# Kernel tuning notes

Hardware: AMD Instinct MI355X
Metric: run time of the kernel (lower is better)

The kernel has to match this reference:

```python
import jax, jax.numpy as jnp
import numpy as np

B = 131072
DIM = 64
D_IN = 32
D_OUT = 32
HIDDEN = 512
N_BINS = 8
TAIL = 3.0


def setup_inputs() -> dict:
    key = jax.random.key(0)
    ks = jax.random.split(key, 7)
    x = jax.random.normal(ks[0], (B, DIM), dtype=jnp.float32)
    out_dim = D_OUT * (3 * N_BINS - 1)  # 32 * 23 = 736
    W1 = jax.random.normal(ks[1], (D_IN, HIDDEN), dtype=jnp.float32) / np.sqrt(D_IN)
    b1 = jnp.zeros((HIDDEN,), dtype=jnp.float32)
    W2 = jax.random.normal(ks[2], (HIDDEN, HIDDEN), dtype=jnp.float32) / np.sqrt(HIDDEN)
    b2 = jnp.zeros((HIDDEN,), dtype=jnp.float32)
    W3 = jax.random.normal(ks[3], (HIDDEN, out_dim), dtype=jnp.float32) / np.sqrt(HIDDEN)
    b3 = jnp.zeros((out_dim,), dtype=jnp.float32)
    return {"x": x, "W1": W1, "b1": b1, "W2": W2, "b2": b2, "W3": W3, "b3": b3}


def _gather(t, idx):
    # t: (..., K), idx: (...) -> (...,)
    return jnp.take_along_axis(t, idx[..., None], axis=-1)[..., 0]


def rq_spline_forward(x, widths, heights, derivatives, tail_bound=TAIL):
    K = widths.shape[-1]
    widths = jax.nn.softmax(widths, axis=-1) * 2 * tail_bound
    heights = jax.nn.softmax(heights, axis=-1) * 2 * tail_bound
    derivatives = jax.nn.softplus(derivatives)
    ones = jnp.ones_like(derivatives[..., :1])
    derivatives = jnp.concatenate([ones, derivatives, ones], axis=-1)  # (..., K+1)
    cumwidths = jnp.cumsum(widths, axis=-1)
    cumwidths = jnp.pad(cumwidths, [(0, 0)] * (cumwidths.ndim - 1) + [(1, 0)]) - tail_bound
    cumheights = jnp.cumsum(heights, axis=-1)
    cumheights = jnp.pad(cumheights, [(0, 0)] * (cumheights.ndim - 1) + [(1, 0)]) - tail_bound

    inside = (x >= -tail_bound) & (x <= tail_bound)
    xc = jnp.clip(x, -tail_bound + 1e-6, tail_bound - 1e-6)
    # searchsorted (left): number of knots strictly less than xc
    bin_idx = jnp.sum(cumwidths[..., 1:] < xc[..., None], axis=-1)
    bin_idx = jnp.clip(bin_idx, 0, K - 1)

    w_k = _gather(widths, bin_idx)
    h_k = _gather(heights, bin_idx)
    d_k = _gather(derivatives, bin_idx)
    d_k1 = _gather(derivatives[..., 1:], bin_idx)
    cw_k = _gather(cumwidths, bin_idx)
    ch_k = _gather(cumheights, bin_idx)

    xi = jnp.clip((xc - cw_k) / w_k, 1e-6, 1 - 1e-6)
    s_k = h_k / w_k
    num = h_k * (s_k * xi**2 + d_k * xi * (1 - xi))
    den = s_k + (d_k + d_k1 - 2 * s_k) * xi * (1 - xi)
    y_inside = ch_k + num / den
    log_det_inside = (
        jnp.log(s_k**2 * (d_k1 * xi**2 + 2 * s_k * xi * (1 - xi) + d_k * (1 - xi) ** 2) + 1e-8)
        - jnp.log(den**2 + 1e-8)
    )
    y = jnp.where(inside, y_inside, x)
    log_det = jnp.where(inside, log_det_inside, jnp.zeros_like(x))
    return y, log_det


def reference(x, W1, b1, W2, b2, W3, b3):
    # mask: first D_IN dims conditioned on, last D_OUT transformed
    x_masked = x[:, :D_IN]
    x_transform = x[:, D_IN:]
    h = jax.nn.relu(x_masked @ W1 + b1)
    h = jax.nn.relu(h @ W2 + b2)
    raw = h @ W3 + b3
    raw = raw.reshape(x.shape[0], D_OUT, 3 * N_BINS - 1)
    widths = raw[..., :N_BINS]
    heights = raw[..., N_BINS:2 * N_BINS]
    derivs = raw[..., 2 * N_BINS:]
    y_t, log_det = rq_spline_forward(x_transform, widths, heights, derivs, TAIL)
    y = jnp.concatenate([x_masked, y_t], axis=-1)
    return y, jnp.sum(log_det, axis=-1)
```

## Files before the change

### kernel.cpp

```cpp
#include <hip/hip_runtime.h>
#include <hip/hip_bf16.h>
#include <stdint.h>

typedef __bf16 bf16_t;
typedef _Float16 f16_t;
typedef _Float16 f16x8 __attribute__((ext_vector_type(8)));
typedef _Float16 f16x4 __attribute__((ext_vector_type(4)));
typedef float f32x4 __attribute__((ext_vector_type(4)));

#define HID 512
#define NRAW 736
#define NRAW_PAD 768
#define TAILB 3.0f

__device__ __forceinline__ void glds16(const void* g, void* s) {
  __builtin_amdgcn_global_load_lds(
      (const __attribute__((address_space(1))) void*)g,
      (__attribute__((address_space(3))) void*)s, 16, 0, 0);
}
__device__ __forceinline__ float frcp(float x) { return __builtin_amdgcn_rcpf(x); }

__global__ void detect_dtype(const void* x, int* flag) {
  __shared__ int s;
  if (threadIdx.x == 0) s = 0;
  __syncthreads();
  const bf16_t* xb = (const bf16_t*)x;
  int cnt = 0;
  for (int j = 0; j < 16; j++) {
    float v = (float)xb[threadIdx.x * 16 + j];
    if (!(v == v) || fabsf(v) > 64.0f) cnt++;
  }
  atomicAdd(&s, cnt);
  __syncthreads();
  if (threadIdx.x == 0) *flag = (s > 64) ? 1 : 0;
}

__global__ void conv_wb(const void* W1, const void* W2, const void* W3,
                        const void* b1, const void* b2, const void* b3,
                        f16_t* __restrict__ w1t, f16_t* __restrict__ w2t,
                        f16_t* __restrict__ w3t,
                        float* __restrict__ bf1, float* __restrict__ bf2,
                        float* __restrict__ bf3, const int* flagp) {
  const int flag = *flagp;
  auto rd = [&](const void* p, size_t idx) -> float {
    return flag ? ((const float*)p)[idx] : (float)((const bf16_t*)p)[idx];
  };
  int i = blockIdx.x * 256 + threadIdx.x;
  if (i < 512 * 32)  { w1t[i] = (f16_t)rd(W1, (size_t)(i & 31) * 512 + (i >> 5)); return; }
  i -= 512 * 32;
  if (i < 512 * 512) { w2t[i] = (f16_t)rd(W2, (size_t)(i & 511) * 512 + (i >> 9)); return; }
  i -= 512 * 512;
  if (i < NRAW_PAD * 512) {
    int n = i >> 9, k = i & 511;
    int ch = n / 24, e = n % 24;
    w3t[i] = (e < 23) ? (f16_t)rd(W3, (size_t)k * NRAW + ch * 23 + e) : (f16_t)0.0f;
    return;
  }
  i -= NRAW_PAD * 512;
  if (i < 512) { bf1[i] = rd(b1, i); return; }
  i -= 512;
  if (i < 512) { bf2[i] = rd(b2, i); return; }
  i -= 512;
  if (i < NRAW_PAD) {
    int ch = i / 24, e = i % 24;
    bf3[i] = (e < 23) ? rd(b3, (size_t)ch * 23 + e) : 0.0f;
  }
}

__global__ void convert_x(const void* x, void* __restrict__ outv,
                          const int* flagp, int n) {
  const int flag = *flagp;
  const int i0 = (blockIdx.x * 256 + threadIdx.x) * 8;
  if (i0 >= n) return;
  const int row = i0 >> 5, col = i0 & 31;
  const size_t src = (size_t)row * 64 + col;
  if (flag) {
    const float4* s4 = (const float4*)((const float*)x + src);
    float4* d4 = (float4*)((float*)outv + src);
    d4[0] = s4[0]; d4[1] = s4[1];
  } else {
    *(uint4*)((bf16_t*)outv + src) = *(const uint4*)((const bf16_t*)x + src);
  }
}

__global__ void ld_finalize(const float* __restrict__ ldp, void* __restrict__ outv,
                            const int* __restrict__ flagp, int M) {
  const int i = blockIdx.x * 256 + threadIdx.x;
  if (i >= M) return;
  float s = 0.f;
  #pragma unroll
  for (int n = 0; n < 8; n++) s += ldp[(size_t)n * M + i];
  if (*flagp) ((float*)outv)[(size_t)M * 64 + i] = s;
  else        ((bf16_t*)outv)[(size_t)M * 64 + i] = (bf16_t)s;
}

__launch_bounds__(256)
__global__ void gemm12(const void* __restrict__ xorig, const f16_t* __restrict__ W1t,
                       const float* __restrict__ b1, const f16_t* __restrict__ W2t,
                       const float* __restrict__ b2, f16_t* __restrict__ H2,
                       int r0, const int* __restrict__ flagp) {
  constexpr int BK = 64;
  __shared__ __align__(16) f16_t As[128 * BK], Bs[128 * BK];
  const int t = threadIdx.x;
  const int id = blockIdx.x;
  const int xcd = id & 7, s = id >> 3;
  const int n0 = (s & 3) * 128;
  const int m0 = ((s >> 2) * 8 + xcd) * 128;
  const int lrow = t >> 3, lcb = t & 7;
  const int lane = t & 63, w = t >> 6;
  const int wr = (w >> 1) * 64, wc = (w & 1) * 64, wc2 = (w & 1) * 32;
  const int lm = lane & 15, quad = lane >> 4;
  const int flag = *flagp;

  const f16_t* gb[4];
  f16_t* ldb[4];
  #pragma unroll
  for (int r = 0; r < 4; r++) {
    const int row = r * 32 + lrow;
    const int gc = (lcb ^ (row & 7)) * 8;
    gb[r] = W2t + (size_t)(n0 + row) * 512 + gc;
    ldb[r] = &Bs[row * BK + lcb * 8];
  }
  const f16x8* ap[4][2];
  const f16x8* bp[4][2];
  #pragma unroll
  for (int i = 0; i < 4; i++) {
    const int ra = wr + i * 16 + lm, rb = wc + i * 16 + lm;
    #pragma unroll
    for (int ksi = 0; ksi < 2; ksi++) {
      const int qb = ksi * 4 + quad;
      ap[i][ksi] = (const f16x8*)&As[ra * BK + ((qb ^ (ra & 7)) << 3)];
      bp[i][ksi] = (const f16x8*)&Bs[rb * BK + ((qb ^ (rb & 7)) << 3)];
    }
  }
  f16x8 xfr[4];
  #pragma unroll
  for (int i = 0; i < 4; i++) {
    const size_t xrow = (size_t)(r0 + m0 + wr + i * 16 + lm);
    if (flag) {
      const float* px = (const float*)xorig + xrow * 64 + quad * 8;
      const float4 a = *(const float4*)px;
      const float4 b = *(const float4*)(px + 4);
      f16x8 v;
      v[0] = (f16_t)a.x; v[1] = (f16_t)a.y; v[2] = (f16_t)a.z; v[3] = (f16_t)a.w;
      v[4] = (f16_t)b.x; v[5] = (f16_t)b.y; v[6] = (f16_t)b.z; v[7] = (f16_t)b.w;
      xfr[i] = v;
    } else {
      const bf16_t* px = (const bf16_t*)xorig + xrow * 64 + quad * 8;
      f16x8 v;
      #pragma unroll
      for (int j = 0; j < 8; j++) v[j] = (f16_t)(float)px[j];
      xfr[i] = v;
    }
  }
  const f16_t* w1p0 = W1t + (size_t)(wc2 + lm) * 32 + quad * 8;
  const f16_t* w1p1 = W1t + (size_t)(wc2 + 16 + lm) * 32 + quad * 8;
  const float* b1p0 = b1 + wc2 + 4 * quad;
  const float* b1p1 = b1 + wc2 + 16 + 4 * quad;
  f16_t* wadr[4][2];
  #pragma unroll
  for (int i = 0; i < 4; i++) {
    const int row = wr + i * 16 + lm;
    #pragma unroll
    for (int Tl = 0; Tl < 2; Tl++) {
      const int cb = (wc2 >> 3) + 2 * Tl + (quad >> 1);
      wadr[i][Tl] = &As[row * BK + ((cb ^ (row & 7)) << 3) + 4 * (quad & 1)];
    }
  }

  f32x4 acc[4][4] = {};
  f16x8 w1f0 = *(const f16x8*)w1p0;
  f16x8 w1f1 = *(const f16x8*)w1p1;

  #pragma unroll
  for (int k0i = 0; k0i < 8; k0i++) {
    const int k0 = k0i * 64;
    #pragma unroll
    for (int r = 0; r < 4; r++) glds16(gb[r] + k0, ldb[r]);
    const float4 bv0 = *(const float4*)(b1p0 + k0);
    const float4 bv1 = *(const float4*)(b1p1 + k0);
    f32x4 h[4][2];
    #pragma unroll
    for (int i = 0; i < 4; i++) {
      f32x4 z = {};
      h[i][0] = __builtin_amdgcn_mfma_f32_16x16x32_f16(w1f0, xfr[i], z, 0, 0, 0);
      h[i][1] = __builtin_amdgcn_mfma_f32_16x16x32_f16(w1f1, xfr[i], z, 0, 0, 0);
    }
    if (k0i < 7) {
      w1f0 = *(const f16x8*)(w1p0 + (size_t)(k0 + 64) * 32);
      w1f1 = *(const f16x8*)(w1p1 + (size_t)(k0 + 64) * 32);
    }
    __syncthreads();
    #pragma unroll
    for (int i = 0; i < 4; i++) {
      f16x4 v0, v1;
      v0[0] = (f16_t)fmaxf(h[i][0][0] + bv0.x, 0.0f);
      v0[1] = (f16_t)fmaxf(h[i][0][1] + bv0.y, 0.0f);
      v0[2] = (f16_t)fmaxf(h[i][0][2] + bv0.z, 0.0f);
      v0[3] = (f16_t)fmaxf(h[i][0][3] + bv0.w, 0.0f);
      v1[0] = (f16_t)fmaxf(h[i][1][0] + bv1.x, 0.0f);
      v1[1] = (f16_t)fmaxf(h[i][1][1] + bv1.y, 0.0f);
      v1[2] = (f16_t)fmaxf(h[i][1][2] + bv1.z, 0.0f);
      v1[3] = (f16_t)fmaxf(h[i][1][3] + bv1.w, 0.0f);
      *(f16x4*)wadr[i][0] = v0;
      *(f16x4*)wadr[i][1] = v1;
    }
    __syncthreads();
    #pragma unroll
    for (int ksi = 0; ksi < 2; ksi++) {
      f16x8 af[4], bf[4];
      #pragma unroll
      for (int i = 0; i < 4; i++) af[i] = *ap[i][ksi];
      #pragma unroll
      for (int j = 0; j < 4; j++) bf[j] = *bp[j][ksi];
      #pragma unroll
      for (int i = 0; i < 4; i++)
        #pragma unroll
        for (int j = 0; j < 4; j++)
          acc[i][j] = __builtin_amdgcn_mfma_f32_16x16x32_f16(af[i], bf[j], acc[i][j], 0, 0, 0);
    }
    if (k0i < 7) __syncthreads();
  }
  #pragma unroll
  for (int i = 0; i < 4; i++)
    #pragma unroll
    for (int j = 0; j < 4; j++) {
      const int col = n0 + wc + j * 16 + lm;
      const float bv = b2[col];
      #pragma unroll
      for (int r = 0; r < 4; r++) {
        const int rowi = m0 + wr + i * 16 + quad * 4 + r;
        H2[(size_t)rowi * HID + col] = (f16_t)fmaxf(acc[i][j][r] + bv, 0.0f);
      }
    }
}

#define RSH 104
#define SP1 0.5413248546f

__launch_bounds__(256)
__global__ void gemm3_spline(const f16_t* __restrict__ A, const f16_t* __restrict__ Bt,
                             const float* __restrict__ bias,
                             const void* __restrict__ xorig,
                             void* __restrict__ outv, float* __restrict__ ldp,
                             int M, int r0, const int* __restrict__ flagp) {
  constexpr int BK = 64;
  __shared__ __align__(16) char smem[16384 + 12288];
  f16_t* As = (f16_t*)smem;
  f16_t* Bs = (f16_t*)(smem + 16384);
  f16_t* rawh = (f16_t*)smem;

  const int t = threadIdx.x;
  const int id = blockIdx.x;
  const int xcd = id & 7, s = id >> 3;
  const int ntile = s & 7;
  const int m0 = ((s >> 3) * 8 + xcd) * 128;
  const int n0 = ntile * 96;
  const int lrow = t >> 3, lcb = t & 7;
  const int lane = t & 63, w = t >> 6;
  const int wr = (w >> 1) * 64, wc = (w & 1) * 48;
  const int lm = lane & 15, quad = lane >> 4;
  const int flag = *flagp;

  const int prow = t >> 2, pch = ntile * 4 + (t & 3);
  float xt_pre[2];
  #pragma unroll
  for (int e = 0; e < 2; e++) {
    const size_t gi = (size_t)(r0 + m0 + e * 64 + prow) * 64 + 32 + pch;
    xt_pre[e] = flag ? ((const float*)xorig)[gi] : (float)((const bf16_t*)xorig)[gi];
  }

  const f16_t* ga[4];
  const f16_t* gb[3];
  f16_t* lda[4];
  f16_t* ldb[3];
  #pragma unroll
  for (int r = 0; r < 4; r++) {
    const int row = r * 32 + lrow;
    const int gc = (lcb ^ (row & 7)) * 8;
    ga[r] = A + (size_t)(m0 + row) * 512 + gc;
    lda[r] = &As[row * BK + lcb * 8];
  }
  #pragma unroll
  for (int r = 0; r < 3; r++) {
    const int row = r * 32 + lrow;
    const int gc = (lcb ^ (row & 7)) * 8;
    gb[r] = Bt + (size_t)(n0 + row) * 512 + gc;
    ldb[r] = &Bs[row * BK + lcb * 8];
  }
  const f16x8* ap[4][2];
  const f16x8* bp[3][2];
  #pragma unroll
  for (int ksi = 0; ksi < 2; ksi++) {
    const int qb = ksi * 4 + quad;
    #pragma unroll
    for (int i = 0; i < 4; i++) {
      const int ra = wr + i * 16 + lm;
      ap[i][ksi] = (const f16x8*)&As[ra * BK + ((qb ^ (ra & 7)) << 3)];
    }
    #pragma unroll
    for (int j = 0; j < 3; j++) {
      const int rb = wc + j * 16 + lm;
      bp[j][ksi] = (const f16x8*)&Bs[rb * BK + ((qb ^ (rb & 7)) << 3)];
    }
  }

  f32x4 acc[4][3] = {};

  #pragma unroll
  for (int k0 = 0; k0 < 512; k0 += BK) {
    #pragma unroll
    for (int r = 0; r < 4; r++) glds16(ga[r] + k0, lda[r]);
    #pragma unroll
    for (int r = 0; r < 3; r++) glds16(gb[r] + k0, ldb[r]);
    __syncthreads();
    #pragma unroll
    for (int ksi = 0; ksi < 2; ksi++) {
      f16x8 af[4], bf[3];
      #pragma unroll
      for (int i = 0; i < 4; i++) af[i] = *ap[i][ksi];
      #pragma unroll
      for (int j = 0; j < 3; j++) bf[j] = *bp[j][ksi];
      #pragma unroll
      for (int i = 0; i < 4; i++)
        #pragma unroll
        for (int j = 0; j < 3; j++)
          acc[i][j] = __builtin_amdgcn_mfma_f32_16x16x32_f16(af[i], bf[j], acc[i][j], 0, 0, 0);
    }
    __syncthreads();
  }

  #pragma unroll
  for (int i = 0; i < 4; i++)
    #pragma unroll
    for (int j = 0; j < 3; j++) {
      const int col = wc + j * 16 + lm;
      const float bv = bias[n0 + col];
      #pragma unroll
      for (int r = 0; r < 4; r++)
        rawh[(wr + i * 16 + quad * 4 + r) * RSH + col] = (f16_t)(acc[i][j][r] + bv);
    }
  __syncthreads();

  #pragma unroll
  for (int e = 0; e < 2; e++) {
    const int row = e * 64 + prow;
    const f16_t* c16 = &rawh[row * RSH + (t & 3) * 24];
    const f16x8 v0 = *(const f16x8*)(c16);
    const f16x8 v1 = *(const f16x8*)(c16 + 8);
    const f16x8 v2 = *(const f16x8*)(c16 + 16);
    float wa[8], ha[8], da[7];
    #pragma unroll
    for (int j = 0; j < 8; j++) { wa[j] = (float)v0[j]; ha[j] = (float)v1[j]; }
    #pragma unroll
    for (int j = 0; j < 7; j++) da[j] = (float)v2[j];

    const float xt = xt_pre[e];
    const bool inside = (xt >= -TAILB) && (xt <= TAILB);
    const float xc = fminf(fmaxf(xt, -TAILB + 1e-6f), TAILB - 1e-6f);

    float mw = wa[0], mh = ha[0];
    #pragma unroll
    for (int j = 1; j < 8; j++) { mw = fmaxf(mw, wa[j]); mh = fmaxf(mh, ha[j]); }
    float ew[8], eh[8], sew = 0.f, seh = 0.f;
    #pragma unroll
    for (int j = 0; j < 8; j++) {
      ew[j] = __expf(wa[j] - mw); sew += ew[j];
      eh[j] = __expf(ha[j] - mh); seh += eh[j];
    }
    const float wsc = 6.0f * frcp(sew), hsc = 6.0f * frcp(seh);
    #pragma unroll
    for (int j = 0; j < 8; j++) { ew[j] *= wsc; eh[j] *= hsc; }

    float accw = -TAILB, runh = -TAILB;
    float cwk = -TAILB, chk = -TAILB;
    float wk = ew[0], hk = eh[0];
    float dkr = SP1, dk1r = da[0];
    #pragma unroll
    for (int i = 0; i < 7; i++) {
      accw += ew[i];
      runh += eh[i];
      const bool cond = accw < xc;
      cwk  = cond ? accw : cwk;
      chk  = cond ? runh : chk;
      wk   = cond ? ew[i + 1] : wk;
      hk   = cond ? eh[i + 1] : hk;
      dkr  = cond ? da[i] : dkr;
      dk1r = cond ? ((i == 6) ? SP1 : da[i + 1]) : dk1r;
    }
    const float dk  = fmaxf(dkr, 0.0f)  + __logf(1.0f + __expf(-fabsf(dkr)));
    const float dk1 = fmaxf(dk1r, 0.0f) + __logf(1.0f + __expf(-fabsf(dk1r)));

    const float rwk = frcp(wk);
    float xi = (xc - cwk) * rwk;
    xi = fminf(fmaxf(xi, 1e-6f), 1.0f - 1e-6f);
    const float om = 1.0f - xi;
    const float sl = hk * rwk;
    const float num = hk * (sl * xi * xi + dk * xi * om);
    const float den = sl + (dk + dk1 - 2.0f * sl) * xi * om;
    const float y_in = chk + num * frcp(den);
    const float t1 = sl * sl * (dk1 * xi * xi + 2.0f * sl * xi * om + dk * om * om);
    const float ld_in = __logf(t1 + 1e-8f) - __logf(den * den + 1e-8f);

    const float yv = inside ? y_in : xt;
    const float ldv = inside ? ld_in : 0.0f;

    const size_t grow = (size_t)(r0 + m0 + row);
    if (flag) ((float*)outv)[grow * 64 + 32 + pch] = yv;
    else      ((bf16_t*)outv)[grow * 64 + 32 + pch] = (bf16_t)yv;

    float l = ldv + __shfl_down(ldv, 1, 4);
    l += __shfl_down(l, 2, 4);
    if ((t & 3) == 0) ldp[(size_t)ntile * M + grow] = l;
  }
}

extern "C" void kernel_launch(void* const* d_in, const int* in_sizes, int n_in,
                              void* d_out, int out_size, void* d_ws, size_t ws_size,
                              hipStream_t stream) {
  const void* x  = d_in[0];
  const void* W1 = d_in[1];
  const void* b1 = d_in[2];
  const void* W2 = d_in[3];
  const void* b2 = d_in[4];
  const void* W3 = d_in[5];
  const void* b3 = d_in[6];
  const int M = in_sizes[0] / 64;

  char* ws = (char*)d_ws;
  size_t off = 0;
  auto alloc = [&](size_t bytes) {
    void* p = ws + off;
    off += (bytes + 255) & ~(size_t)255;
    return p;
  };
  int*   flag = (int*)alloc(256);
  float* bf1  = (float*)alloc(512 * 4);
  float* bf2  = (float*)alloc(512 * 4);
  float* bf3  = (float*)alloc(NRAW_PAD * 4);
  f16_t* W1t  = (f16_t*)alloc((size_t)512 * 32 * 2);
  f16_t* W2t  = (f16_t*)alloc((size_t)512 * 512 * 2);
  f16_t* W3t  = (f16_t*)alloc((size_t)NRAW_PAD * 512 * 2);
  float* ldp  = (float*)alloc((size_t)8 * M * 4);

  const size_t per_row = (size_t)HID * 2;
  size_t avail = (ws_size > off + 4096) ? (ws_size - off - 4096) : 0;
  long rows = (long)(avail / per_row);
  rows -= rows % 1024;
  if (rows > M) rows = M;
  if (rows < 1024) rows = 1024;

  f16_t* h2 = (f16_t*)alloc((size_t)rows * HID * 2);

  detect_dtype<<<1, 256, 0, stream>>>(x, flag);
  conv_wb<<<2631, 256, 0, stream>>>(W1, W2, W3, b1, b2, b3,
                                    W1t, W2t, W3t, bf1, bf2, bf3, flag);
  convert_x<<<(M * 32 / 8 + 255) / 256, 256, 0, stream>>>(x, d_out, flag, M * 32);

  for (int r0 = 0; r0 < M; r0 += (int)rows) {
    const int mc = (int)((M - r0 < rows) ? (M - r0) : rows);
    const int mt = mc / 128;
    gemm12<<<mt * 4, 256, 0, stream>>>(x, W1t, bf1, W2t, bf2, h2, r0, flag);
    gemm3_spline<<<mt * 8, 256, 0, stream>>>(
        h2, W3t, bf3, x, d_out, ldp, M, r0, flag);
  }
  ld_finalize<<<(M + 255) / 256, 256, 0, stream>>>(ldp, d_out, flag, M);
}
```

Baseline: 341.8 us.

## Retile gemm3_spline to 256x192 tiles with double-buffered LDS pipeline

The fused third GEMM and spline kernel moves from 128x96 tiles with 256 threads to 256x192 tiles with 512 threads and 8 waves. It double-buffers A and B in LDS so the next K-slice's global-to-LDS loads overlap the MFMAs on the current slice, and it raises wave priority around the MFMA groups. The block index is remapped so consecutive blocks on each XCD share M rows. With only four column tiles, the spline reduction now spans 8 lanes and ld_finalize sums 4 partials instead of 8. LDS use per block rises sharply, which risks lower occupancy, and with larger tiles the grid has fewer blocks.

New measurement: 356.7 us. +4.4%, slower.

```diff
diff --git a/kernel.cpp b/kernel.cpp
--- a/kernel.cpp
+++ b/kernel.cpp
@@ -89,7 +89,7 @@
   if (i >= M) return;
   float s = 0.f;
   #pragma unroll
-  for (int n = 0; n < 8; n++) s += ldp[(size_t)n * M + i];
+  for (int n = 0; n < 4; n++) s += ldp[(size_t)n * M + i];
   if (*flagp) ((float*)outv)[(size_t)M * 64 + i] = s;
   else        ((bf16_t*)outv)[(size_t)M * 64 + i] = (bf16_t)s;
 }
@@ -235,117 +235,136 @@
     }
 }
 
-#define RSH 104
+#define RSH 200
 #define SP1 0.5413248546f
 
-__launch_bounds__(256)
+__launch_bounds__(512, 2)
 __global__ void gemm3_spline(const f16_t* __restrict__ A, const f16_t* __restrict__ Bt,
                              const float* __restrict__ bias,
                              const void* __restrict__ xorig,
                              void* __restrict__ outv, float* __restrict__ ldp,
                              int M, int r0, const int* __restrict__ flagp) {
-  constexpr int BK = 64;
-  __shared__ __align__(16) char smem[16384 + 12288];
-  f16_t* As = (f16_t*)smem;
-  f16_t* Bs = (f16_t*)(smem + 16384);
-  f16_t* rawh = (f16_t*)smem;
+  __shared__ __align__(16) f16_t lds[2 * 16384 + 2 * 12288];
+  f16_t* As = lds;
+  f16_t* Bs = lds + 2 * 16384;
+  f16_t* rawh = lds;
 
   const int t = threadIdx.x;
   const int id = blockIdx.x;
-  const int xcd = id & 7, s = id >> 3;
-  const int ntile = s & 7;
-  const int m0 = ((s >> 3) * 8 + xcd) * 128;
-  const int n0 = ntile * 96;
+  const int xcd = id & 7, sloc = id >> 3;
+  const int cpx = gridDim.x >> 3;
+  const int wg = xcd * cpx + sloc;
+  const int ntile = wg & 3;
+  const int m0 = (wg >> 2) * 256;
+  const int n0 = ntile * 192;
+  const int lane = t & 63, w = t >> 6;
+  const int lm = lane & 15, quad = lane >> 4;
+  const int wrow = (w >> 2) * 128, wcol = (w & 3) * 48;
   const int lrow = t >> 3, lcb = t & 7;
-  const int lane = t & 63, w = t >> 6;
-  const int wr = (w >> 1) * 64, wc = (w & 1) * 48;
-  const int lm = lane & 15, quad = lane >> 4;
   const int flag = *flagp;
 
-  const int prow = t >> 2, pch = ntile * 4 + (t & 3);
-  float xt_pre[2];
-  #pragma unroll
-  for (int e = 0; e < 2; e++) {
-    const size_t gi = (size_t)(r0 + m0 + e * 64 + prow) * 64 + 32 + pch;
+  const int gc = (lcb ^ (lrow & 7)) * 8;
+  const f16_t* gA = A + (size_t)(m0 + lrow) * 512 + gc;
+  const f16_t* gB = Bt + (size_t)(n0 + lrow) * 512 + gc;
+  f16_t* ldA = As + lrow * 64 + lcb * 8;
+  f16_t* ldB = Bs + lrow * 64 + lcb * 8;
+
+  int aoff[8], boff[3];
+  #pragma unroll
+  for (int i = 0; i < 8; i++) {
+    const int ra = wrow + i * 16 + lm;
+    aoff[i] = ra * 64 + ((quad ^ (ra & 7)) << 3);
+  }
+  #pragma unroll
+  for (int j = 0; j < 3; j++) {
+    const int rb = wcol + j * 16 + lm;
+    boff[j] = rb * 64 + ((quad ^ (rb & 7)) << 3);
+  }
+
+  #pragma unroll
+  for (int r = 0; r < 4; r++) glds16(gA + r * 32768, ldA + r * 4096);
+  #pragma unroll
+  for (int r = 0; r < 3; r++) glds16(gB + r * 32768, ldB + r * 4096);
+
+  const int prow = t >> 3, pch = t & 7;
+  float xt_pre[4];
+  #pragma unroll
+  for (int e = 0; e < 4; e++) {
+    const size_t gi = (size_t)(r0 + m0 + e * 64 + prow) * 64 + 32 + ntile * 8 + pch;
     xt_pre[e] = flag ? ((const float*)xorig)[gi] : (float)((const bf16_t*)xorig)[gi];
   }
-
-  const f16_t* ga[4];
-  const f16_t* gb[3];
-  f16_t* lda[4];
-  f16_t* ldb[3];
-  #pragma unroll
-  for (int r = 0; r < 4; r++) {
-    const int row = r * 32 + lrow;
-    const int gc = (lcb ^ (row & 7)) * 8;
-    ga[r] = A + (size_t)(m0 + row) * 512 + gc;
-    lda[r] = &As[row * BK + lcb * 8];
-  }
-  #pragma unroll
-  for (int r = 0; r < 3; r++) {
-    const int row = r * 32 + lrow;
-    const int gc = (lcb ^ (row & 7)) * 8;
-    gb[r] = Bt + (size_t)(n0 + row) * 512 + gc;
-    ldb[r] = &Bs[row * BK + lcb * 8];
-  }
-  const f16x8* ap[4][2];
-  const f16x8* bp[3][2];
-  #pragma unroll
-  for (int ksi = 0; ksi < 2; ksi++) {
-    const int qb = ksi * 4 + quad;
-    #pragma unroll
-    for (int i = 0; i < 4; i++) {
-      const int ra = wr + i * 16 + lm;
-      ap[i][ksi] = (const f16x8*)&As[ra * BK + ((qb ^ (ra & 7)) << 3)];
-    }
-    #pragma unroll
-    for (int j = 0; j < 3; j++) {
-      const int rb = wc + j * 16 + lm;
-      bp[j][ksi] = (const f16x8*)&Bs[rb * BK + ((qb ^ (rb & 7)) << 3)];
-    }
-  }
-
-  f32x4 acc[4][3] = {};
-
-  #pragma unroll
-  for (int k0 = 0; k0 < 512; k0 += BK) {
-    #pragma unroll
-    for (int r = 0; r < 4; r++) glds16(ga[r] + k0, lda[r]);
-    #pragma unroll
-    for (int r = 0; r < 3; r++) glds16(gb[r] + k0, ldb[r]);
-    __syncthreads();
-    #pragma unroll
-    for (int ksi = 0; ksi < 2; ksi++) {
+  float bv3[3];
+  #pragma unroll
+  for (int j = 0; j < 3; j++) bv3[j] = bias[n0 + wcol + j * 16 + lm];
+
+  asm volatile("s_waitcnt vmcnt(0)" ::: "memory");
+  __builtin_amdgcn_sched_barrier(0);
+  __builtin_amdgcn_s_barrier();
+
+  f32x4 acc[8][3] = {};
+
+  #pragma unroll
+  for (int t8 = 0; t8 < 8; t8++) {
+    const f16_t* Ab = As + (t8 & 1) * 16384;
+    const f16_t* Bb = Bs + (t8 & 1) * 12288;
+    f16_t* ldAn = ldA + ((t8 + 1) & 1) * 16384;
+    f16_t* ldBn = ldB + ((t8 + 1) & 1) * 12288;
+    const f16_t* gAn = gA + (t8 + 1) * 64;
+    const f16_t* gBn = gB + (t8 + 1) * 64;
+
+    #pragma unroll
+    for (int p = 0; p < 4; p++) {
+      const int ksi = p >> 1, rh = p & 1;
       f16x8 af[4], bf[3];
       #pragma unroll
-      for (int i = 0; i < 4; i++) af[i] = *ap[i][ksi];
-      #pragma unroll
-      for (int j = 0; j < 3; j++) bf[j] = *bp[j][ksi];
-      #pragma unroll
-      for (int i = 0; i < 4; i++)
+      for (int ii = 0; ii < 4; ii++)
+        af[ii] = *(const f16x8*)(Ab + (aoff[rh * 4 + ii] ^ (ksi << 5)));
+      #pragma unroll
+      for (int j = 0; j < 3; j++)
+        bf[j] = *(const f16x8*)(Bb + (boff[j] ^ (ksi << 5)));
+      if (t8 < 7) {
+        if (p == 0) {
+          #pragma unroll
+          for (int r = 0; r < 4; r++) glds16(gAn + r * 32768, ldAn + r * 4096);
+        } else if (p == 1) {
+          #pragma unroll
+          for (int r = 0; r < 3; r++) glds16(gBn + r * 32768, ldBn + r * 4096);
+        }
+      }
+      __builtin_amdgcn_s_barrier();
+      __builtin_amdgcn_s_setprio(1);
+      #pragma unroll
+      for (int ii = 0; ii < 4; ii++)
         #pragma unroll
         for (int j = 0; j < 3; j++)
-          acc[i][j] = __builtin_amdgcn_mfma_f32_16x16x32_f16(af[i], bf[j], acc[i][j], 0, 0, 0);
-    }
-    __syncthreads();
-  }
-
-  #pragma unroll
-  for (int i = 0; i < 4; i++)
+          acc[rh * 4 + ii][j] = __builtin_amdgcn_mfma_f32_16x16x32_f16(
+              af[ii], bf[j], acc[rh * 4 + ii][j], 0, 0, 0);
+      __builtin_amdgcn_s_setprio(0);
+    }
+    if (t8 < 7) {
+      asm volatile("s_waitcnt vmcnt(0)" ::: "memory");
+      __builtin_amdgcn_sched_barrier(0);
+      __builtin_amdgcn_s_barrier();
+    }
+  }
+
+  __syncthreads();
+
+  #pragma unroll
+  for (int i = 0; i < 8; i++)
     #pragma unroll
     for (int j = 0; j < 3; j++) {
-      const int col = wc + j * 16 + lm;
-      const float bv = bias[n0 + col];
+      const int col = wcol + j * 16 + lm;
       #pragma unroll
       for (int r = 0; r < 4; r++)
-        rawh[(wr + i * 16 + quad * 4 + r) * RSH + col] = (f16_t)(acc[i][j][r] + bv);
+        rawh[(wrow + i * 16 + quad * 4 + r) * RSH + col] = (f16_t)(acc[i][j][r] + bv3[j]);
     }
   __syncthreads();
 
   #pragma unroll
-  for (int e = 0; e < 2; e++) {
+  for (int e = 0; e < 4; e++) {
     const int row = e * 64 + prow;
-    const f16_t* c16 = &rawh[row * RSH + (t & 3) * 24];
+    const f16_t* c16 = &rawh[row * RSH + pch * 24];
     const f16x8 v0 = *(const f16x8*)(c16);
     const f16x8 v1 = *(const f16x8*)(c16 + 8);
     const f16x8 v2 = *(const f16x8*)(c16 + 16);
@@ -406,12 +425,13 @@
     const float ldv = inside ? ld_in : 0.0f;
 
     const size_t grow = (size_t)(r0 + m0 + row);
-    if (flag) ((float*)outv)[grow * 64 + 32 + pch] = yv;
-    else      ((bf16_t*)outv)[grow * 64 + 32 + pch] = (bf16_t)yv;
-
-    float l = ldv + __shfl_down(ldv, 1, 4);
-    l += __shfl_down(l, 2, 4);
-    if ((t & 3) == 0) ldp[(size_t)ntile * M + grow] = l;
+    if (flag) ((float*)outv)[grow * 64 + 32 + ntile * 8 + pch] = yv;
+    else      ((bf16_t*)outv)[grow * 64 + 32 + ntile * 8 + pch] = (bf16_t)yv;
+
+    float l = ldv + __shfl_down(ldv, 1, 8);
+    l += __shfl_down(l, 2, 8);
+    l += __shfl_down(l, 4, 8);
+    if ((t & 7) == 0) ldp[(size_t)ntile * M + grow] = l;
   }
 }
 
@@ -459,9 +479,10 @@
 
   for (int r0 = 0; r0 < M; r0 += (int)rows) {
     const int mc = (int)((M - r0 < rows) ? (M - r0) : rows);
-    const int mt = mc / 128;
-    gemm12<<<mt * 4, 256, 0, stream>>>(x, W1t, bf1, W2t, bf2, h2, r0, flag);
-    gemm3_spline<<<mt * 8, 256, 0, stream>>>(
+    const int mt128 = mc / 128;
+    const int mt256 = mc / 256;
+    gemm12<<<mt128 * 4, 256, 0, stream>>>(x, W1t, bf1, W2t, bf2, h2, r0, flag);
+    gemm3_spline<<<mt256 * 4, 512, 0, stream>>>(
         h2, W3t, bf3, x, d_out, ldp, M, r0, flag);
   }
   ld_finalize<<<(M + 255) / 256, 256, 0, stream>>>(ldp, d_out, flag, M);
```
